# Kernel tuning notes

Hardware: AMD Instinct MI355X
Metric: run time of the kernel (lower is better)

## Reference

```python
import jax, jax.numpy as jnp
import numpy as np

N, D = 256, 512
DIST_W, ANGLE_W = 1.0, 2.0
EPS_PD = 1e-6    # F.pairwise_distance eps (added to the difference)
EPS_COS = 1e-8   # F.cosine_similarity eps (denominator floor)
CLAMP = 1e-7     # acos clamp margin


def _smooth_l1(x):
    # F.smooth_l1_loss with beta=1.0, elementwise (reduction handled by caller)
    ax = jnp.abs(x)
    return jnp.where(ax < 1.0, 0.5 * ax * ax, ax - 0.5)


def _pairwise_dist(E):
    # Faithful to the looped version: dist[i,j] = ||e_i - e_j + eps|| for i<j,
    # mirrored to the lower triangle, zero diagonal.
    diff = E[:, None, :] - E[None, :, :] + EPS_PD          # [n, n, d]
    d = jnp.sqrt(jnp.sum(diff * diff, axis=-1))            # [n, n]
    upper = jnp.triu(d, k=1)
    return upper + upper.T


def _angles(E):
    # ang[j, i, k] = angle at vertex j between (e_i - e_j) and (e_k - e_j)
    Dv = E[None, :, :] - E[:, None, :]                     # Dv[j, a] = e_a - e_j
    norms = jnp.sqrt(jnp.sum(Dv * Dv, axis=-1))            # [n, n]
    dots = jnp.einsum('jad,jbd->jab', Dv, Dv)              # [n, n, n]
    denom = jnp.maximum(norms[:, :, None] * norms[:, None, :], EPS_COS)
    cos = jnp.clip(dots / denom, -1.0 + CLAMP, 1.0 - CLAMP)
    return jnp.arccos(cos)


def setup_inputs() -> dict:
    key = jax.random.key(0)
    k1, k2 = jax.random.split(key)
    return {
        'student_embeddings': jax.random.normal(k1, (N, D), dtype=jnp.float32),
        'teacher_embeddings': jax.random.normal(k2, (N, D), dtype=jnp.float32),
    }


def reference(student_embeddings, teacher_embeddings):
    # distance-wise loss: smooth_l1 mean over the full n x n matrix
    ds = _pairwise_dist(student_embeddings)
    dt = _pairwise_dist(teacher_embeddings)
    distance_loss = jnp.mean(_smooth_l1(ds - dt))

    # angle-wise loss: mean over triplets i<j<k (vertex at j)
    n = student_embeddings.shape[0]
    ang_s = _angles(student_embeddings)
    ang_t = _angles(teacher_embeddings)
    idx = jnp.arange(n)
    # mask[j, i, k] = (i < j) & (j < k)
    mask = (idx[None, :, None] < idx[:, None, None]) & (idx[:, None, None] < idx[None, None, :])
    count = n * (n - 1) * (n - 2) // 6
    angle_loss = jnp.sum(_smooth_l1(ang_s - ang_t) * mask) / count

    total_loss = DIST_W * distance_loss + ANGLE_W * angle_loss
    return (total_loss, distance_loss, angle_loss)
```

## Files before the change

kernel.cpp:

```cpp
#include <hip/hip_runtime.h>
#include <math.h>

#define N 256
#define D 512
#define SPLIT 4

using f32x4  = __attribute__((ext_vector_type(4))) float;
using bf16x8 = __attribute__((ext_vector_type(8))) short;

__device__ __forceinline__ short f2bf(float f) {
    __bf16 h = (__bf16)f;
    return __builtin_bit_cast(short, h);
}

__device__ __forceinline__ float smooth_l1(float x) {
    float ax = fabsf(x);
    return ax < 1.f ? 0.5f * ax * ax : ax - 0.5f;
}

__device__ __forceinline__ float acos_fast(float x) {
    float ax = fabsf(x);
    float p = -0.0187293f;
    p = p * ax + 0.0742610f;
    p = p * ax - 0.2121144f;
    p = p * ax + 1.5707288f;
    float v = sqrtf(1.f - ax) * p;
    return x < 0.f ? 3.14159265358979f - v : v;
}

__global__ __launch_bounds__(64) void gram_kernel(const float* __restrict__ Es,
                                                  const float* __restrict__ Et,
                                                  float2* __restrict__ G2,
                                                  float* __restrict__ acc) {
    const int lane = threadIdx.x;
    if (blockIdx.x == 0 && blockIdx.y == 0 && blockIdx.z == 0 && lane == 0) {
        acc[0] = 0.f;
        acc[1] = 0.f;
    }
    if (blockIdx.y > blockIdx.x) return;

    const float* E = blockIdx.z ? Et : Es;
    const int m = lane & 15, quad = lane >> 4;
    const int baseA = (blockIdx.y * 16 + m) * D + quad * 8;
    const int baseB = (blockIdx.x * 16 + m) * D + quad * 8;

    f32x4 c = {0.f, 0.f, 0.f, 0.f};
#pragma unroll
    for (int k0 = 0; k0 < D; k0 += 32) {
        float4 alo = *(const float4*)&E[baseA + k0];
        float4 ahi = *(const float4*)&E[baseA + k0 + 4];
        float4 blo = *(const float4*)&E[baseB + k0];
        float4 bhi = *(const float4*)&E[baseB + k0 + 4];
        bf16x8 a, b;
        a[0] = f2bf(alo.x); a[1] = f2bf(alo.y); a[2] = f2bf(alo.z); a[3] = f2bf(alo.w);
        a[4] = f2bf(ahi.x); a[5] = f2bf(ahi.y); a[6] = f2bf(ahi.z); a[7] = f2bf(ahi.w);
        b[0] = f2bf(blo.x); b[1] = f2bf(blo.y); b[2] = f2bf(blo.z); b[3] = f2bf(blo.w);
        b[4] = f2bf(bhi.x); b[5] = f2bf(bhi.y); b[6] = f2bf(bhi.z); b[7] = f2bf(bhi.w);
        c = __builtin_amdgcn_mfma_f32_16x16x32_bf16(a, b, c, 0, 0, 0);
    }

    const int col = blockIdx.x * 16 + m;
    const bool mirror = blockIdx.y < blockIdx.x;
#pragma unroll
    for (int r = 0; r < 4; ++r) {
        const int row = blockIdx.y * 16 + quad * 4 + r;
        ((float*)&G2[row * N + col])[blockIdx.z] = c[r];
        if (mirror)
            ((float*)&G2[col * N + row])[blockIdx.z] = c[r];
    }
}

__global__ __launch_bounds__(256) void angle_dist_kernel(const float2* __restrict__ G2,
                                                         float* __restrict__ acc) {
    const int j = blockIdx.x + 1;
    const int tid = threadIdx.x;
    __shared__ float4 stv[N];
    __shared__ float2 red[4];
    const float2 gjj = G2[j * N + j];
    const float Gsjj = gjj.x, Gtjj = gjj.y;

    float distp = 0.f;
    {
        const int a = tid;
        float2 gaj = G2[a * N + j];
        float2 gaa = G2[a * N + a];
        float n2s = gaa.x - 2.f * gaj.x + Gsjj;
        float n2t = gaa.y - 2.f * gaj.y + Gtjj;
        float rs = (a == j) ? 0.f : rsqrtf(n2s);
        float rt = (a == j) ? 0.f : rsqrtf(n2t);
        stv[a] = make_float4(gaj.x, rs, gaj.y, rt);
        if (blockIdx.y == 0 && a < j)
            distp = smooth_l1(n2s * rs - n2t * rt);
    }
    __syncthreads();

    const int nk = 255 - j;
    const int npairs = j * nk;
    const float inv_nk = 1.0f / (float)nk;
    const float lo = -0.99999994f;
    const float hi = 0.99999994f;

    float anglep = 0.f;
    for (int p = blockIdx.y * 256 + tid; p < npairs; p += 256 * SPLIT) {
        int i = (int)((float)p * inv_nk);
        int rem = p - i * nk;
        if (rem < 0) { --i; rem += nk; }
        else if (rem >= nk) { ++i; rem -= nk; }
        const int k = j + 1 + rem;
        float4 si = stv[i], sk = stv[k];
        float2 gik = G2[i * N + k];
        float dots = gik.x - si.x - sk.x + Gsjj;
        float dott = gik.y - si.z - sk.z + Gtjj;
        float coss = fminf(fmaxf(dots * (si.y * sk.y), lo), hi);
        float cost = fminf(fmaxf(dott * (si.w * sk.w), lo), hi);
        anglep += smooth_l1(acos_fast(coss) - acos_fast(cost));
    }

    float vx = distp, vy = anglep;
#pragma unroll
    for (int off = 32; off > 0; off >>= 1) {
        vx += __shfl_down(vx, off);
        vy += __shfl_down(vy, off);
    }
    if ((tid & 63) == 0) red[tid >> 6] = make_float2(vx, vy);
    __syncthreads();
    if (tid == 0) {
        float rx = red[0].x + red[1].x + red[2].x + red[3].x;
        float ry = red[0].y + red[1].y + red[2].y + red[3].y;
        atomicAdd(&acc[1], ry);
        if (blockIdx.y == 0) atomicAdd(&acc[0], rx);
    }
}

__global__ void finalize_kernel(const float* __restrict__ acc,
                                float* __restrict__ out) {
    float dl = 2.f * acc[0] / (float)(N * N);
    float al = acc[1] / (float)(N * (N - 1) * (N - 2) / 6);
    out[0] = 1.0f * dl + 2.0f * al;
    out[1] = dl;
    out[2] = al;
}

extern "C" void kernel_launch(void* const* d_in, const int* in_sizes, int n_in,
                              void* d_out, int out_size, void* d_ws, size_t ws_size,
                              hipStream_t stream) {
    const float* Es = (const float*)d_in[0];
    const float* Et = (const float*)d_in[1];
    float* out = (float*)d_out;
    float* ws = (float*)d_ws;

    float* acc = ws;
    float2* G2 = (float2*)(ws + 64);

    gram_kernel<<<dim3(16, 16, 2), 64, 0, stream>>>(Es, Et, G2, acc);
    angle_dist_kernel<<<dim3(N - 1, SPLIT), 256, 0, stream>>>(G2, acc);
    finalize_kernel<<<1, 1, 0, stream>>>(acc, out);
}
```

Baseline: 84.77 us.

## Use 32x32 register tiles and triangular block indexing in Gram kernel

Result: no change. 84.21 us (-0.7%).

```diff
diff --git a/kernel.cpp b/kernel.cpp
--- a/kernel.cpp
+++ b/kernel.cpp
@@ -11,6 +11,13 @@
 __device__ __forceinline__ short f2bf(float f) {
     __bf16 h = (__bf16)f;
     return __builtin_bit_cast(short, h);
+}
+
+__device__ __forceinline__ bf16x8 cvt8(float4 lo, float4 hi) {
+    bf16x8 v;
+    v[0] = f2bf(lo.x); v[1] = f2bf(lo.y); v[2] = f2bf(lo.z); v[3] = f2bf(lo.w);
+    v[4] = f2bf(hi.x); v[5] = f2bf(hi.y); v[6] = f2bf(hi.z); v[7] = f2bf(hi.w);
+    return v;
 }
 
 __device__ __forceinline__ float smooth_l1(float x) {
@@ -33,40 +40,56 @@
                                                   float2* __restrict__ G2,
                                                   float* __restrict__ acc) {
     const int lane = threadIdx.x;
-    if (blockIdx.x == 0 && blockIdx.y == 0 && blockIdx.z == 0 && lane == 0) {
+    const int t = blockIdx.x;
+    if (t == 0 && blockIdx.z == 0 && lane == 0) {
         acc[0] = 0.f;
         acc[1] = 0.f;
     }
-    if (blockIdx.y > blockIdx.x) return;
+    int bx = (int)((sqrtf(8.f * (float)t + 1.f) - 1.f) * 0.5f);
+    if ((bx + 1) * (bx + 2) / 2 <= t) ++bx;
+    else if (bx * (bx + 1) / 2 > t) --bx;
+    const int by = t - bx * (bx + 1) / 2;
 
     const float* E = blockIdx.z ? Et : Es;
     const int m = lane & 15, quad = lane >> 4;
-    const int baseA = (blockIdx.y * 16 + m) * D + quad * 8;
-    const int baseB = (blockIdx.x * 16 + m) * D + quad * 8;
+    const int baseA0 = (by * 32 + m) * D + quad * 8;
+    const int baseA1 = baseA0 + 16 * D;
+    const int baseB0 = (bx * 32 + m) * D + quad * 8;
+    const int baseB1 = baseB0 + 16 * D;
 
-    f32x4 c = {0.f, 0.f, 0.f, 0.f};
+    f32x4 c00 = {0.f, 0.f, 0.f, 0.f};
+    f32x4 c01 = c00, c10 = c00, c11 = c00;
 #pragma unroll
     for (int k0 = 0; k0 < D; k0 += 32) {
-        float4 alo = *(const float4*)&E[baseA + k0];
-        float4 ahi = *(const float4*)&E[baseA + k0 + 4];
-        float4 blo = *(const float4*)&E[baseB + k0];
-        float4 bhi = *(const float4*)&E[baseB + k0 + 4];
-        bf16x8 a, b;
-        a[0] = f2bf(alo.x); a[1] = f2bf(alo.y); a[2] = f2bf(alo.z); a[3] = f2bf(alo.w);
-        a[4] = f2bf(ahi.x); a[5] = f2bf(ahi.y); a[6] = f2bf(ahi.z); a[7] = f2bf(ahi.w);
-        b[0] = f2bf(blo.x); b[1] = f2bf(blo.y); b[2] = f2bf(blo.z); b[3] = f2bf(blo.w);
-        b[4] = f2bf(bhi.x); b[5] = f2bf(bhi.y); b[6] = f2bf(bhi.z); b[7] = f2bf(bhi.w);
-        c = __builtin_amdgcn_mfma_f32_16x16x32_bf16(a, b, c, 0, 0, 0);
+        bf16x8 a0 = cvt8(*(const float4*)&E[baseA0 + k0], *(const float4*)&E[baseA0 + k0 + 4]);
+        bf16x8 a1 = cvt8(*(const float4*)&E[baseA1 + k0], *(const float4*)&E[baseA1 + k0 + 4]);
+        bf16x8 b0 = cvt8(*(const float4*)&E[baseB0 + k0], *(const float4*)&E[baseB0 + k0 + 4]);
+        bf16x8 b1 = cvt8(*(const float4*)&E[baseB1 + k0], *(const float4*)&E[baseB1 + k0 + 4]);
+        c00 = __builtin_amdgcn_mfma_f32_16x16x32_bf16(a0, b0, c00, 0, 0, 0);
+        c01 = __builtin_amdgcn_mfma_f32_16x16x32_bf16(a0, b1, c01, 0, 0, 0);
+        c10 = __builtin_amdgcn_mfma_f32_16x16x32_bf16(a1, b0, c10, 0, 0, 0);
+        c11 = __builtin_amdgcn_mfma_f32_16x16x32_bf16(a1, b1, c11, 0, 0, 0);
     }
 
-    const int col = blockIdx.x * 16 + m;
-    const bool mirror = blockIdx.y < blockIdx.x;
+    const bool mirror = by < bx;
+    const int rowb = by * 32 + quad * 4;
+    const int colb = bx * 32 + m;
+    const int z = blockIdx.z;
 #pragma unroll
-    for (int r = 0; r < 4; ++r) {
-        const int row = blockIdx.y * 16 + quad * 4 + r;
-        ((float*)&G2[row * N + col])[blockIdx.z] = c[r];
-        if (mirror)
-            ((float*)&G2[col * N + row])[blockIdx.z] = c[r];
+    for (int sa = 0; sa < 2; ++sa) {
+#pragma unroll
+        for (int sb = 0; sb < 2; ++sb) {
+            const f32x4 c = (sa == 0) ? (sb == 0 ? c00 : c01)
+                                      : (sb == 0 ? c10 : c11);
+            const int col = colb + sb * 16;
+#pragma unroll
+            for (int r = 0; r < 4; ++r) {
+                const int row = rowb + sa * 16 + r;
+                ((float*)&G2[row * N + col])[z] = c[r];
+                if (mirror)
+                    ((float*)&G2[col * N + row])[z] = c[r];
+            }
+        }
     }
 }
 
@@ -152,7 +175,7 @@
     float* acc = ws;
     float2* G2 = (float2*)(ws + 64);
 
-    gram_kernel<<<dim3(16, 16, 2), 64, 0, stream>>>(Es, Et, G2, acc);
+    gram_kernel<<<dim3(36, 1, 2), 64, 0, stream>>>(Es, Et, G2, acc);
     angle_dist_kernel<<<dim3(N - 1, SPLIT), 256, 0, stream>>>(G2, acc);
     finalize_kernel<<<1, 1, 0, stream>>>(acc, out);
 }
```
